# Optimization experiments

Hardware: AMD Instinct MI355X
Metric: run time of the kernel (lower is better)

The kernel has to match this reference:

```python
import jax, jax.numpy as jnp
import numpy as np

INPUT_SIZE, HIDDEN, OUT = 2, 32, 1

def setup_inputs() -> dict:
    key = jax.random.key(0)
    ks = jax.random.split(key, 8)
    B, T = 2048, 512
    s_ih = 1.0 / np.sqrt(HIDDEN)
    return {
        "x": jax.random.normal(ks[0], (B, T, INPUT_SIZE), dtype=jnp.float32),
        "W_ih": jax.random.uniform(ks[1], (4 * HIDDEN, INPUT_SIZE), minval=-s_ih, maxval=s_ih, dtype=jnp.float32),
        "W_hh": jax.random.uniform(ks[2], (4 * HIDDEN, HIDDEN), minval=-s_ih, maxval=s_ih, dtype=jnp.float32),
        "b_ih": jax.random.uniform(ks[3], (4 * HIDDEN,), minval=-s_ih, maxval=s_ih, dtype=jnp.float32),
        "b_hh": jax.random.uniform(ks[4], (4 * HIDDEN,), minval=-s_ih, maxval=s_ih, dtype=jnp.float32),
        "W_fc": jax.random.uniform(ks[5], (OUT, HIDDEN), minval=-s_ih, maxval=s_ih, dtype=jnp.float32),
        "b_fc": jax.random.uniform(ks[6], (OUT,), minval=-s_ih, maxval=s_ih, dtype=jnp.float32),
    }

def _lstm(x, W_ih, W_hh, b_ih, b_hh):
    # x: [B, T, I]; PyTorch gate order: i, f, g, o
    B, T, _ = x.shape
    H = W_hh.shape[1]
    # precompute input projections for all timesteps: [T, B, 4H]
    xp = jnp.einsum('bti,gi->tbg', x, W_ih) + (b_ih + b_hh)

    def step(carry, xp_t):
        h, c = carry
        gates = xp_t + h @ W_hh.T  # [B, 4H]
        i, f, g, o = jnp.split(gates, 4, axis=-1)
        i = jax.nn.sigmoid(i)
        f = jax.nn.sigmoid(f)
        g = jnp.tanh(g)
        o = jax.nn.sigmoid(o)
        c = f * c + i * g
        h = o * jnp.tanh(c)
        return (h, c), h

    h0 = jnp.zeros((B, H), dtype=x.dtype)
    c0 = jnp.zeros((B, H), dtype=x.dtype)
    _, hs = jax.lax.scan(step, (h0, c0), xp)  # hs: [T, B, H]
    return jnp.transpose(hs, (1, 0, 2))  # [B, T, H]

def reference(x, W_ih, W_hh, b_ih, b_hh, W_fc, b_fc):
    lstm_out = _lstm(x, W_ih, W_hh, b_ih, b_hh)  # [B, T, H]
    return lstm_out @ W_fc.T + b_fc  # [B, T, OUT]
```

## Files before the change

kernel.cpp:

```cpp
#include <hip/hip_runtime.h>


#define BB 2048
#define TT 512
#define HH 32
#define CHUNK 64
#define HROW 33

#define LOG2E 1.44269504088896340736f

typedef float v2f __attribute__((ext_vector_type(2)));
typedef float v4f __attribute__((ext_vector_type(4)));
typedef unsigned int v2u __attribute__((ext_vector_type(2)));

__device__ __forceinline__ float sigm2(float xs) {
    return __builtin_amdgcn_rcpf(1.0f + __builtin_amdgcn_exp2f(-xs));
}

__global__ __launch_bounds__(256, 2) void lstm_fused_kernel(
    const float* __restrict__ x,
    const float* __restrict__ W_ih,
    const float* __restrict__ W_hh,
    const float* __restrict__ b_ih,
    const float* __restrict__ b_hh,
    const float* __restrict__ W_fc,
    const float* __restrict__ b_fc,
    float* __restrict__ out)
{
    __shared__ float lds_x[4 * TT * 2];
    __shared__ float lds_h[4 * CHUNK * HROW];
    __shared__ __align__(16) float lds_bc[4][64];

    const int lane = threadIdx.x & 63;
    const int wv   = threadIdx.x >> 6;
    const int b    = blockIdx.x * 4 + wv;
    const bool low = (lane < 32);

    {
        const float4* xg = (const float4*)(x + (size_t)b * TT * 2);
        float4* xs = (float4*)(lds_x + wv * TT * 2);
        #pragma unroll
        for (int r = 0; r < 4; ++r) xs[r * 64 + lane] = xg[r * 64 + lane];
    }

    const int rlo = lane;
    const int rhi = lane + 64;
    const float sl = LOG2E;
    const float sh = low ? 2.0f * LOG2E : LOG2E;

    const v2f wihl = ((const v2f*)W_ih)[rlo] * sl;
    const v2f wihh = ((const v2f*)W_ih)[rhi] * sh;
    const float bl = (b_ih[rlo] + b_hh[rlo]) * sl;
    const float bh = (b_ih[rhi] + b_hh[rhi]) * sh;

    v2f wloq[HH / 2], whiq[HH / 2];
    #pragma unroll
    for (int k = 0; k < HH / 2; ++k) {
        wloq[k] = ((const v2f*)(W_hh + rlo * HH))[k] * sl;
        whiq[k] = ((const v2f*)(W_hh + rhi * HH))[k] * sh;
    }

    float wfc[HH];
    #pragma unroll
    for (int u = 0; u < HH; ++u) wfc[u] = W_fc[u];
    const float bfc = b_fc[0];

    const float Aa = low ?  4.0f * LOG2E : 1.0f;
    const float Bb = low ? -2.0f * LOG2E : 0.0f;

    float c = 0.0f;

    float* out_b = out + (size_t)b * TT;
    const v4f* xw4 = (const v4f*)(lds_x + wv * TT * 2);
    float* hb  = lds_h + wv * CHUNK * HROW;
    float* bcw = lds_bc[wv];
    const v4f* bcr = (const v4f*)bcw;

    bcw[lane] = 0.0f;

    const v2f binitL = {bl, 0.0f};
    const v2f binitH = {bh, 0.0f};

    float* wr = low ? (bcw + lane) : (hb + (lane - 32));
    const int winc = low ? 0 : HROW;

    #pragma unroll 1
    for (int ch = 0; ch < TT / CHUNK; ++ch) {
        #pragma unroll 1
        for (int uu = 0; uu < CHUNK; uu += 2) {
            v4f xq = xw4[(ch * CHUNK + uu) >> 1];

            #pragma unroll
            for (int s = 0; s < 2; ++s) {
                v4f hq[8];
                #pragma unroll
                for (int q = 0; q < 8; ++q) hq[q] = bcr[q];

                v2f xt = s ? (v2f){xq.z, xq.w} : (v2f){xq.x, xq.y};

                v2f aL0 = __builtin_elementwise_fma(xt, wihl, binitL);
                v2f aH0 = __builtin_elementwise_fma(xt, wihh, binitH);
                v2f aL1 = {0.0f, 0.0f};
                v2f aH1 = {0.0f, 0.0f};

                #pragma unroll
                for (int k = 0; k < HH / 2; ++k) {
                    v2f hp = (k & 1)
                        ? __builtin_shufflevector(hq[k >> 1], hq[k >> 1], 2, 3)
                        : __builtin_shufflevector(hq[k >> 1], hq[k >> 1], 0, 1);
                    if (k < HH / 4) {
                        aL0 = __builtin_elementwise_fma(hp, wloq[k], aL0);
                        aH0 = __builtin_elementwise_fma(hp, whiq[k], aH0);
                    } else {
                        aL1 = __builtin_elementwise_fma(hp, wloq[k], aL1);
                        aH1 = __builtin_elementwise_fma(hp, whiq[k], aH1);
                    }
                }
                v2f aL = aL0 + aL1;
                v2f aH = aH0 + aH1;
                float glo = aL.x + aL.y;
                float ghi = aH.x + aH.y;

                float alo = sigm2(glo);
                float shi = sigm2(ghi);
                float ahi = fmaf(Aa, shi, Bb);

                v2u r1 = __builtin_amdgcn_permlane32_swap(
                    __float_as_uint(alo), __float_as_uint(alo), false, false);
                v2u r2 = __builtin_amdgcn_permlane32_swap(
                    __float_as_uint(ahi), __float_as_uint(ahi), false, false);
                float fv = __uint_as_float(r1.y);
                float iv = __uint_as_float(r1.x);
                float ov = __uint_as_float(r2.y);
                float gv = __uint_as_float(r2.x);

                float ig = iv * gv;
                c = fmaf(fv, c, ig);

                float rr  = sigm2(c);
                float ov2 = ov + ov;
                float hnew = fmaf(ov2, rr, -ov);

                *wr = hnew;
                wr += winc;
            }
        }

        wr -= winc * CHUNK;

        float acc = bfc;
        const float* row = hb + lane * HROW;
        #pragma unroll
        for (int u = 0; u < HH; ++u)
            acc = fmaf(row[u], wfc[u], acc);
        out_b[ch * CHUNK + lane] = acc;
    }
}

extern "C" void kernel_launch(void* const* d_in, const int* in_sizes, int n_in,
                              void* d_out, int out_size, void* d_ws, size_t ws_size,
                              hipStream_t stream) {
    const float* x    = (const float*)d_in[0];
    const float* W_ih = (const float*)d_in[1];
    const float* W_hh = (const float*)d_in[2];
    const float* b_ih = (const float*)d_in[3];
    const float* b_hh = (const float*)d_in[4];
    const float* W_fc = (const float*)d_in[5];
    const float* b_fc = (const float*)d_in[6];
    float* out = (float*)d_out;

    dim3 grid(BB / 4);
    dim3 block(256);
    lstm_fused_kernel<<<grid, block, 0, stream>>>(x, W_ih, W_hh, b_ih, b_hh,
                                                  W_fc, b_fc, out);
}
```

Before: 213.2 us.

## Interleave two batch sequences per wavefront to hide recurrence latency

Each wavefront now runs two independent batch rows, alternating their recurrent steps so one sequence's dependent chain (LDS write, readback, FMAs, transcendentals, permlane swaps) can overlap the other's. The x staging in LDS is dropped in favour of direct global loads prefetched one 4-step group ahead, and each gate row is remapped so a lane holds matching rows. Chunk size shrinks to 32 with padded rows, the grid is halved, and launch bounds drop to one block per SIMD pair. This trades occupancy and more register pressure for instruction-level parallelism inside each wave.

Measured after the change: 247.1 us. 1.16x slower.

```diff
diff --git a/kernel.cpp b/kernel.cpp
--- a/kernel.cpp
+++ b/kernel.cpp
@@ -4,8 +4,9 @@
 #define BB 2048
 #define TT 512
 #define HH 32
-#define CHUNK 64
-#define HROW 33
+#define CHUNK 32
+#define ROWF 36
+#define WS (2 * CHUNK * ROWF + 4)
 
 #define LOG2E 1.44269504088896340736f
 
@@ -17,7 +18,7 @@
     return __builtin_amdgcn_rcpf(1.0f + __builtin_amdgcn_exp2f(-xs));
 }
 
-__global__ __launch_bounds__(256, 2) void lstm_fused_kernel(
+__global__ __launch_bounds__(256, 1) void lstm_fused_kernel(
     const float* __restrict__ x,
     const float* __restrict__ W_ih,
     const float* __restrict__ W_hh,
@@ -27,24 +28,17 @@
     const float* __restrict__ b_fc,
     float* __restrict__ out)
 {
-    __shared__ float lds_x[4 * TT * 2];
-    __shared__ float lds_h[4 * CHUNK * HROW];
-    __shared__ __align__(16) float lds_bc[4][64];
+    __shared__ __align__(16) float lds_h[4][WS];
 
     const int lane = threadIdx.x & 63;
     const int wv   = threadIdx.x >> 6;
-    const int b    = blockIdx.x * 4 + wv;
+    const int j    = lane & 31;
     const bool low = (lane < 32);
-
-    {
-        const float4* xg = (const float4*)(x + (size_t)b * TT * 2);
-        float4* xs = (float4*)(lds_x + wv * TT * 2);
-        #pragma unroll
-        for (int r = 0; r < 4; ++r) xs[r * 64 + lane] = xg[r * 64 + lane];
-    }
-
-    const int rlo = lane;
-    const int rhi = lane + 64;
+    const int bA   = blockIdx.x * 8 + wv * 2;
+    const int bB   = bA + 1;
+
+    const int rlo = j + (low ? 0 : HH);
+    const int rhi = j + (low ? 2 * HH : 3 * HH);
     const float sl = LOG2E;
     const float sh = low ? 2.0f * LOG2E : LOG2E;
 
@@ -53,11 +47,11 @@
     const float bl = (b_ih[rlo] + b_hh[rlo]) * sl;
     const float bh = (b_ih[rhi] + b_hh[rhi]) * sh;
 
-    v2f wloq[HH / 2], whiq[HH / 2];
+    v2f wlo[HH / 2], whi[HH / 2];
     #pragma unroll
     for (int k = 0; k < HH / 2; ++k) {
-        wloq[k] = ((const v2f*)(W_hh + rlo * HH))[k] * sl;
-        whiq[k] = ((const v2f*)(W_hh + rhi * HH))[k] * sh;
+        wlo[k] = ((const v2f*)(W_hh + rlo * HH))[k] * sl;
+        whi[k] = ((const v2f*)(W_hh + rhi * HH))[k] * sh;
     }
 
     float wfc[HH];
@@ -67,93 +61,128 @@
 
     const float Aa = low ?  4.0f * LOG2E : 1.0f;
     const float Bb = low ? -2.0f * LOG2E : 0.0f;
-
-    float c = 0.0f;
-
-    float* out_b = out + (size_t)b * TT;
-    const v4f* xw4 = (const v4f*)(lds_x + wv * TT * 2);
-    float* hb  = lds_h + wv * CHUNK * HROW;
-    float* bcw = lds_bc[wv];
-    const v4f* bcr = (const v4f*)bcw;
-
-    bcw[lane] = 0.0f;
-
     const v2f binitL = {bl, 0.0f};
     const v2f binitH = {bh, 0.0f};
 
-    float* wr = low ? (bcw + lane) : (hb + (lane - 32));
-    const int winc = low ? 0 : HROW;
+    float cA = 0.0f, cB = 0.0f;
+
+    float* hbA = &lds_h[wv][0];
+    float* hbB = &lds_h[wv][CHUNK * ROWF];
+
+    hbA[(CHUNK - 1) * ROWF + j] = 0.0f;
+    hbB[(CHUNK - 1) * ROWF + j] = 0.0f;
+
+    v4f hqA[8], hqB[8];
+    {
+        const v4f* ra = (const v4f*)(hbA + (CHUNK - 1) * ROWF);
+        const v4f* rb = (const v4f*)(hbB + (CHUNK - 1) * ROWF);
+        #pragma unroll
+        for (int q = 0; q < 8; ++q) hqA[q] = ra[q];
+        #pragma unroll
+        for (int q = 0; q < 8; ++q) hqB[q] = rb[q];
+    }
+
+    float* wrA = hbA + j;
+    float* wrB = hbB + j;
+
+    const float* xpA = x + (size_t)bA * (TT * 2);
+    const float* xpB = x + (size_t)bB * (TT * 2);
+    v4f xA0 = *(const v4f*)(xpA),     xA1 = *(const v4f*)(xpA + 4);
+    v4f xB0 = *(const v4f*)(xpB),     xB1 = *(const v4f*)(xpB + 4);
+
+    float* outp = (low ? (out + (size_t)bA * TT) : (out + (size_t)bB * TT)) + j;
+    const float* frow = (low ? hbA : hbB) + j * ROWF;
+
+    auto step = [&](const v4f (&hq)[8], v2f xt, float& c) -> float {
+        v2f aL0 = __builtin_elementwise_fma(xt, wihl, binitL);
+        v2f aH0 = __builtin_elementwise_fma(xt, wihh, binitH);
+        v2f aL1, aH1;
+        #pragma unroll
+        for (int k = 0; k < HH / 2; ++k) {
+            v2f hp = (k & 1)
+                ? __builtin_shufflevector(hq[k >> 1], hq[k >> 1], 2, 3)
+                : __builtin_shufflevector(hq[k >> 1], hq[k >> 1], 0, 1);
+            if (k < HH / 4) {
+                aL0 = __builtin_elementwise_fma(hp, wlo[k], aL0);
+                aH0 = __builtin_elementwise_fma(hp, whi[k], aH0);
+            } else if (k == HH / 4) {
+                aL1 = hp * wlo[k];
+                aH1 = hp * whi[k];
+            } else {
+                aL1 = __builtin_elementwise_fma(hp, wlo[k], aL1);
+                aH1 = __builtin_elementwise_fma(hp, whi[k], aH1);
+            }
+        }
+        v2f aL = aL0 + aL1;
+        v2f aH = aH0 + aH1;
+        float glo = aL.x + aL.y;
+        float ghi = aH.x + aH.y;
+
+        float alo = sigm2(glo);
+        float ahi = fmaf(Aa, sigm2(ghi), Bb);
+
+        v2u r1 = __builtin_amdgcn_permlane32_swap(
+            __float_as_uint(alo), __float_as_uint(alo), false, false);
+        v2u r2 = __builtin_amdgcn_permlane32_swap(
+            __float_as_uint(ahi), __float_as_uint(ahi), false, false);
+        float fv = __uint_as_float(r1.y);
+        float iv = __uint_as_float(r1.x);
+        float ov = __uint_as_float(r2.y);
+        float gv = __uint_as_float(r2.x);
+
+        c = fmaf(fv, c, iv * gv);
+        float rr  = sigm2(c);
+        float ov2 = ov + ov;
+        return fmaf(ov2, rr, -ov);
+    };
 
     #pragma unroll 1
     for (int ch = 0; ch < TT / CHUNK; ++ch) {
         #pragma unroll 1
-        for (int uu = 0; uu < CHUNK; uu += 2) {
-            v4f xq = xw4[(ch * CHUNK + uu) >> 1];
+        for (int g = 0; g < CHUNK / 4; ++g) {
+            const int t0 = ch * CHUNK + g * 4;
+            const float* nxa = (t0 + 4 < TT) ? (xpA + (t0 + 4) * 2) : xpA;
+            const float* nxb = (t0 + 4 < TT) ? (xpB + (t0 + 4) * 2) : xpB;
+            v4f nA0 = *(const v4f*)(nxa), nA1 = *(const v4f*)(nxa + 4);
+            v4f nB0 = *(const v4f*)(nxb), nB1 = *(const v4f*)(nxb + 4);
 
             #pragma unroll
-            for (int s = 0; s < 2; ++s) {
-                v4f hq[8];
-                #pragma unroll
-                for (int q = 0; q < 8; ++q) hq[q] = bcr[q];
-
-                v2f xt = s ? (v2f){xq.z, xq.w} : (v2f){xq.x, xq.y};
-
-                v2f aL0 = __builtin_elementwise_fma(xt, wihl, binitL);
-                v2f aH0 = __builtin_elementwise_fma(xt, wihh, binitH);
-                v2f aL1 = {0.0f, 0.0f};
-                v2f aH1 = {0.0f, 0.0f};
-
-                #pragma unroll
-                for (int k = 0; k < HH / 2; ++k) {
-                    v2f hp = (k & 1)
-                        ? __builtin_shufflevector(hq[k >> 1], hq[k >> 1], 2, 3)
-                        : __builtin_shufflevector(hq[k >> 1], hq[k >> 1], 0, 1);
-                    if (k < HH / 4) {
-                        aL0 = __builtin_elementwise_fma(hp, wloq[k], aL0);
-                        aH0 = __builtin_elementwise_fma(hp, whiq[k], aH0);
-                    } else {
-                        aL1 = __builtin_elementwise_fma(hp, wloq[k], aL1);
-                        aH1 = __builtin_elementwise_fma(hp, whiq[k], aH1);
-                    }
+            for (int s = 0; s < 4; ++s) {
+                v2f xtA, xtB;
+                if      (s == 0) { xtA = (v2f){xA0.x, xA0.y}; xtB = (v2f){xB0.x, xB0.y}; }
+                else if (s == 1) { xtA = (v2f){xA0.z, xA0.w}; xtB = (v2f){xB0.z, xB0.w}; }
+                else if (s == 2) { xtA = (v2f){xA1.x, xA1.y}; xtB = (v2f){xB1.x, xB1.y}; }
+                else             { xtA = (v2f){xA1.z, xA1.w}; xtB = (v2f){xB1.z, xB1.w}; }
+
+                {
+                    float hnew = step(hqA, xtA, cA);
+                    *wrA = hnew;
+                    const v4f* r = (const v4f*)(wrA - j);
+                    #pragma unroll
+                    for (int q = 0; q < 8; ++q) hqA[q] = r[q];
+                    wrA += ROWF;
                 }
-                v2f aL = aL0 + aL1;
-                v2f aH = aH0 + aH1;
-                float glo = aL.x + aL.y;
-                float ghi = aH.x + aH.y;
-
-                float alo = sigm2(glo);
-                float shi = sigm2(ghi);
-                float ahi = fmaf(Aa, shi, Bb);
-
-                v2u r1 = __builtin_amdgcn_permlane32_swap(
-                    __float_as_uint(alo), __float_as_uint(alo), false, false);
-                v2u r2 = __builtin_amdgcn_permlane32_swap(
-                    __float_as_uint(ahi), __float_as_uint(ahi), false, false);
-                float fv = __uint_as_float(r1.y);
-                float iv = __uint_as_float(r1.x);
-                float ov = __uint_as_float(r2.y);
-                float gv = __uint_as_float(r2.x);
-
-                float ig = iv * gv;
-                c = fmaf(fv, c, ig);
-
-                float rr  = sigm2(c);
-                float ov2 = ov + ov;
-                float hnew = fmaf(ov2, rr, -ov);
-
-                *wr = hnew;
-                wr += winc;
+                {
+                    float hnew = step(hqB, xtB, cB);
+                    *wrB = hnew;
+                    const v4f* r = (const v4f*)(wrB - j);
+                    #pragma unroll
+                    for (int q = 0; q < 8; ++q) hqB[q] = r[q];
+                    wrB += ROWF;
+                }
             }
+            xA0 = nA0; xA1 = nA1; xB0 = nB0; xB1 = nB1;
         }
 
-        wr -= winc * CHUNK;
+        wrA -= CHUNK * ROWF;
+        wrB -= CHUNK * ROWF;
 
         float acc = bfc;
-        const float* row = hb + lane * HROW;
         #pragma unroll
         for (int u = 0; u < HH; ++u)
-            acc = fmaf(row[u], wfc[u], acc);
-        out_b[ch * CHUNK + lane] = acc;
+            acc = fmaf(frow[u], wfc[u], acc);
+        *outp = acc;
+        outp += CHUNK;
     }
 }
 
@@ -169,7 +198,7 @@
     const float* b_fc = (const float*)d_in[6];
     float* out = (float*)d_out;
 
-    dim3 grid(BB / 4);
+    dim3 grid(BB / 8);
     dim3 block(256);
     lstm_fused_kernel<<<grid, block, 0, stream>>>(x, W_ih, W_hh, b_ih, b_hh,
                                                   W_fc, b_fc, out);
```
